# Optimization experiments

Measured on AMD Instinct MI355X. Metric: run time of the kernel, lower is better.

The kernel has to match this reference:

```python
import jax, jax.numpy as jnp
import numpy as np
from jax import lax

YXS = [(100, 250), (250, 250), (400, 250)]
HWS = [(50, 400), (50, 400), (50, 400)]
RATIO = 0.8
RCNN_THRES = 0.25
YOLO_THRES = 0.45
NMS_THRES = 0.4


def setup_inputs() -> dict:
    key = jax.random.key(0)
    ks = jax.random.split(key, 6)
    img = jax.random.uniform(ks[0], (1, 3, 500, 500), dtype=jnp.float32)
    patch0 = jax.random.normal(ks[1], (3, 50, 400), dtype=jnp.float32)
    patch1 = jax.random.normal(ks[2], (3, 50, 400), dtype=jnp.float32)
    patch2 = jax.random.normal(ks[3], (3, 50, 400), dtype=jnp.float32)
    rcnn_probs = jax.random.uniform(ks[4], (6144, 81), dtype=jnp.float32)
    boxes = jax.random.uniform(ks[5], (6144, 6), dtype=jnp.float32)
    return {"img": img, "patch0": patch0, "patch1": patch1, "patch2": patch2,
            "rcnn_probs": rcnn_probs, "boxes": boxes}


def _iou_matrix(b):
    # b: [M,4] center format (x, y, w, h) -> pairwise IoU [M,M]
    x1 = b[:, 0] - b[:, 2] * 0.5
    x2 = b[:, 0] + b[:, 2] * 0.5
    y1 = b[:, 1] - b[:, 3] * 0.5
    y2 = b[:, 1] + b[:, 3] * 0.5
    iw = jnp.maximum(jnp.minimum(x2[:, None], x2[None, :]) - jnp.maximum(x1[:, None], x1[None, :]), 0.0)
    ih = jnp.maximum(jnp.minimum(y2[:, None], y2[None, :]) - jnp.maximum(y1[:, None], y1[None, :]), 0.0)
    inter = iw * ih
    area = b[:, 2] * b[:, 3]
    union = area[:, None] + area[None, :] - inter
    return inter / jnp.maximum(union, 1e-12)


def _box_loss(c5, c4, mask):
    # per-box clamp/log loss on cls_conf (c5) and det_conf (c4), masked sum
    s = 1.0 / (0.5 - YOLO_THRES)
    l = (-jnp.clip((c5 - YOLO_THRES) * s, 0.0, 1.0) * jnp.log(1.0 - c5 + 0.01)
         - jnp.clip((c4 - YOLO_THRES) * s, 0.0, 1.0) * jnp.log(1.0 - c4 + 0.01))
    return jnp.sum(jnp.where(mask, l, 0.0))


def reference(img, patch0, patch1, patch2, rcnn_probs, boxes):
    # --- patch blending ---
    for (y, x), (h, w), p in zip(YXS, HWS, (patch0, patch1, patch2)):
        img = img.at[0, :, y - h // 2:y - h // 2 + h, x - w // 2:x - w // 2 + w].add(p)
    # clamp-violation penalty: (-img[img<0]).sum() + (img[img>1]-1).sum()
    p_loss = jnp.sum(jnp.maximum(-img, 0.0)) + jnp.sum(jnp.maximum(img - 1.0, 0.0))
    img = jnp.clip(img, 0.0, 1.0)

    # --- rcnn postprocessing loss ---
    prob = jnp.max(rcnn_probs[:, :-1], axis=-1)
    rmask = prob > RCNN_THRES
    b_prob = rcnn_probs[:, -1]
    r_loss = -jnp.sum(jnp.where(rmask, jnp.log(b_prob + 0.001), 0.0))
    r_loss += -jnp.sum(jnp.where(rmask,
                                 jnp.clip((prob - RCNN_THRES) / (0.3 - RCNN_THRES), 0.0, 1.0)
                                 * jnp.log(1.0 - prob + 0.001), 0.0))

    # --- yolo per-box loss + greedy IoU-NMS loss ---
    conf = boxes[:, 4]
    valid = conf > YOLO_THRES
    b_loss = _box_loss(boxes[:, 5], conf, valid)

    M = boxes.shape[0]
    order = jnp.argsort(-conf)
    sb = boxes[order]          # sorted by det_conf desc
    sv = valid[order]
    iou = _iou_matrix(sb[:, :4])  # [M,M]
    idx = jnp.arange(M)

    def body(keep, i):
        sup = (iou[i] > NMS_THRES) & (idx > i) & keep[i]
        return keep & ~sup, None

    keep, _ = lax.scan(body, sv, idx)
    b_nms_loss = _box_loss(sb[:, 5], sb[:, 4], keep)

    b_cnt = jnp.sum(valid.astype(jnp.float32))
    b_nms_cnt = jnp.maximum(jnp.sum(keep.astype(jnp.float32)), 1.0)
    yolo_loss = b_loss + b_nms_loss * (b_cnt / b_nms_cnt)

    loss = r_loss * RATIO + yolo_loss + p_loss
    return loss
```

## Files before the change

### kernel.cpp

```cpp
#include <hip/hip_runtime.h>
#include <hip/hip_bf16.h>
#include <stdint.h>

#define RCNN_THRES 0.25f
#define YOLO_THRES 0.45f
#define NMS_THRES  0.4f

#define M_BOXES 6144
#define NWORDS  96
#define SORT_N  4096

#define RK_BLOCKS 96
#define PL_BLOCKS 733
#define RL_BLOCKS 384
#define BL_BLOCKS 6
#define P_ELEMS  750000
#define MB_BLOCKS 1024

typedef unsigned long long u64;

__device__ inline float wave_sum(float v) {
#pragma unroll
    for (int o = 32; o > 0; o >>= 1) v += __shfl_xor(v, o);
    return v;
}
__device__ inline float wave_max(float v) {
#pragma unroll
    for (int o = 32; o > 0; o >>= 1) v = fmaxf(v, __shfl_xor(v, o));
    return v;
}

__device__ inline u64 readlane_u64(u64 v, int l) {
    unsigned lo = (unsigned)__builtin_amdgcn_readlane((int)(unsigned)v, l);
    unsigned hi = (unsigned)__builtin_amdgcn_readlane((int)(unsigned)(v >> 32), l);
    return ((u64)hi << 32) | (u64)lo;
}

__device__ inline float box_loss_term(float c5, float c4) {
    float a = fminf(fmaxf((c5 - YOLO_THRES) * 20.0f, 0.0f), 1.0f);
    float b = fminf(fmaxf((c4 - YOLO_THRES) * 20.0f, 0.0f), 1.0f);
    return -a * logf(1.0f - c5 + 0.01f) - b * logf(1.0f - c4 + 0.01f);
}

__device__ inline bool iou_gt(float x1a, float y1a, float x2a, float y2a, float aa,
                              float x1b, float y1b, float x2b, float y2b, float ab) {
    float iw = fmaxf(fminf(x2a, x2b) - fmaxf(x1a, x1b), 0.0f);
    float ih = fmaxf(fminf(y2a, y2b) - fmaxf(y1a, y1b), 0.0f);
    float inter = iw * ih;
    float uni = aa + ab - inter;
    return (inter / fmaxf(uni, 1e-12f)) > NMS_THRES;
}

__device__ inline u64 vw_word(int w, int nv) {
    int rem = nv - (w << 6);
    if (rem >= 64) return ~0ull;
    if (rem <= 0) return 0ull;
    return (1ull << rem) - 1ull;
}

__global__ __launch_bounds__(1024) void sort_and_losses(
    const float* __restrict__ boxes,
    const float* __restrict__ img, const float* __restrict__ p0,
    const float* __restrict__ p1, const float* __restrict__ p2,
    const float* __restrict__ probs,
    float* __restrict__ sx1, float* __restrict__ sy1,
    float* __restrict__ sx2, float* __restrict__ sy2,
    float* __restrict__ sarea, float* __restrict__ sconf, float* __restrict__ sc5,
    int* __restrict__ nvp, float* __restrict__ acc) {
    const int bid = blockIdx.x;
    const int tid = threadIdx.x, lane = tid & 63, wid = tid >> 6;

    if (bid < RK_BLOCKS) {
        __shared__ u64 KL[M_BOXES];
        __shared__ float cred[16];
        float myvalid = 0.0f;
#pragma unroll
        for (int s = 0; s < 6; ++s) {
            int p = tid + s * 1024;
            float conf = boxes[p * 6 + 4];
            u64 key = 0ull;
            if (conf > YOLO_THRES) {
                key = ((u64)__float_as_uint(conf) << 13) | (u64)(8191 - p);
                myvalid += 1.0f;
            }
            KL[p] = key;
        }
        __syncthreads();
        if (bid == 0) {
            float c = wave_sum(myvalid);
            if (lane == 0) cred[wid] = c;
            __syncthreads();
            if (tid == 0) {
                float t = 0.0f;
#pragma unroll
                for (int k = 0; k < 16; ++k) t += cred[k];
                *nvp = (int)(t + 0.5f);
            }
        }
        const int box = bid * 64 + (tid >> 4);
        const int seg = tid & 15;
        const u64 mykey = KL[box];
        int cnt = 0;
        for (int i = seg; i < M_BOXES; i += 16)
            cnt += (KL[i] > mykey) ? 1 : 0;
#pragma unroll
        for (int o = 1; o < 16; o <<= 1) cnt += __shfl_xor(cnt, o);
        if (seg == 0 && mykey != 0ull) {
            int rank = cnt;
            if (rank < SORT_N) {
                const float* b6 = boxes + box * 6;
                float x = b6[0], y = b6[1], wd = b6[2], ht = b6[3];
                sx1[rank] = x - wd * 0.5f;
                sx2[rank] = x + wd * 0.5f;
                sy1[rank] = y - ht * 0.5f;
                sy2[rank] = y + ht * 0.5f;
                sarea[rank] = wd * ht;
                sconf[rank] = b6[4];
                sc5[rank] = b6[5];
            }
        }
        return;
    }

    __shared__ float fred[32];
    if (bid < RK_BLOCKS + PL_BLOCKS) {
        int e = (bid - RK_BLOCKS) * 1024 + tid;
        float local = 0.0f;
        if (e < P_ELEMS) {
            float v = img[e];
            int c = e / 250000;
            int rem = e - c * 250000;
            int y = rem / 500;
            int x = rem - y * 500;
            if (x >= 50 && x < 450) {
                int px = x - 50;
                if (y >= 75 && y < 125)       v += p0[c * 20000 + (y - 75) * 400 + px];
                else if (y >= 225 && y < 275) v += p1[c * 20000 + (y - 225) * 400 + px];
                else if (y >= 375 && y < 425) v += p2[c * 20000 + (y - 375) * 400 + px];
            }
            local = fmaxf(-v, 0.0f) + fmaxf(v - 1.0f, 0.0f);
        }
        local = wave_sum(local);
        if (lane == 0) fred[wid] = local;
        __syncthreads();
        if (tid == 0) {
            float t = 0.0f;
#pragma unroll
            for (int k = 0; k < 16; ++k) t += fred[k];
            atomicAdd(&acc[0], t);
        }
    } else if (bid < RK_BLOCKS + PL_BLOCKS + RL_BLOCKS) {
        int row = (bid - RK_BLOCKS - PL_BLOCKS) * 16 + wid;
        const float* pr = probs + row * 81;
        float m = pr[lane];
        if (lane < 16) m = fmaxf(m, pr[64 + lane]);
        m = wave_max(m);
        float t = 0.0f;
        if (lane == 0 && m > RCNN_THRES) {
            float bp = pr[80];
            float cl = fminf(fmaxf((m - RCNN_THRES) * (1.0f / (0.3f - RCNN_THRES)), 0.0f), 1.0f);
            t = -logf(bp + 0.001f) - cl * logf(1.0f - m + 0.001f);
        }
        if (lane == 0) fred[wid] = t;
        __syncthreads();
        if (tid == 0) {
            float s = 0.0f;
#pragma unroll
            for (int k = 0; k < 16; ++k) s += fred[k];
            atomicAdd(&acc[1], s);
        }
    } else {
        int i = (bid - RK_BLOCKS - PL_BLOCKS - RL_BLOCKS) * 1024 + tid;
        float l = 0.0f, cnt = 0.0f;
        if (i < M_BOXES) {
            float conf = boxes[i * 6 + 4];
            if (conf > YOLO_THRES) {
                l = box_loss_term(boxes[i * 6 + 5], conf);
                cnt = 1.0f;
            }
        }
        l = wave_sum(l);
        cnt = wave_sum(cnt);
        if (lane == 0) { fred[wid] = l; fred[16 + wid] = cnt; }
        __syncthreads();
        if (tid == 0) {
            float tl = 0.0f, tc = 0.0f;
#pragma unroll
            for (int k = 0; k < 16; ++k) { tl += fred[k]; tc += fred[16 + k]; }
            atomicAdd(&acc[2], tl);
            atomicAdd(&acc[3], tc);
        }
    }
}

__global__ __launch_bounds__(256) void build_mask(
    const float* __restrict__ sx1, const float* __restrict__ sy1,
    const float* __restrict__ sx2, const float* __restrict__ sy2,
    const float* __restrict__ sarea, const int* __restrict__ nvp,
    u64* __restrict__ mask) {
    const int lane = threadIdx.x & 63, wid = threadIdx.x >> 6;
    const int nv = *nvp;
    int row = blockIdx.x * 4 + wid;
    if (row >= nv) return;
    const int nwa = (nv + 63) >> 6;
    float rx1 = sx1[row], ry1 = sy1[row], rx2 = sx2[row], ry2 = sy2[row];
    float ra = sarea[row];
    u64* mrow = mask + (size_t)row * NWORDS;
    for (int w = row >> 6; w < nwa; ++w) {
        int j = w * 64 + lane;
        bool pred = (j > row) && (j < nv) &&
                    iou_gt(rx1, ry1, rx2, ry2, ra,
                           sx1[j], sy1[j], sx2[j], sy2[j], sarea[j]);
        u64 bits = __ballot(pred);
        if (lane == 0) mrow[w] = bits;
    }
}

__global__ __launch_bounds__(512) void nms_walk(
    const float* __restrict__ acc, const int* __restrict__ nvp,
    const u64* __restrict__ mask,
    const float* __restrict__ sconf, const float* __restrict__ sc5,
    float* __restrict__ out) {
    __shared__ u64 SLICE[2][1024];
    __shared__ u64 SUPC[8][NWORDS];
    __shared__ u64 KW[NWORDS];
    __shared__ float fred[16];

    const int tid = threadIdx.x, lane = tid & 63, wid = tid >> 6;
    const int nv = *nvp;
    const int nwa = (nv + 63) >> 6;
    const int ngrp = (nwa + 3) >> 2;

    for (int i = tid; i < 8 * NWORDS; i += 512) ((u64*)SUPC)[i] = 0ull;
    for (int i = tid; i < NWORDS; i += 512) KW[i] = 0ull;
    {
        int r = tid >> 1, h = tid & 1;
        ulonglong2 m = *(const ulonglong2*)(mask + (size_t)r * NWORDS + 2 * h);
        *(ulonglong2*)&SLICE[0][r * 4 + 2 * h] = m;
    }
    __syncthreads();

    for (int g = 0; g < ngrp; ++g) {
        const int W = 4 * g;
        const int buf = g & 1;

        ulonglong2 stg{};
        const bool do_stage = (g + 1 < ngrp);
        if (do_stage) {
            int r = tid >> 1, h = tid & 1;
            stg = *(const ulonglong2*)(mask +
                    (size_t)((g + 1) * 256 + r) * NWORDS + (4 * (g + 1) + 2 * h));
        }

        if (wid == 0) {
            const u64* SL = SLICE[buf];
            ulonglong2 S0lo = *(const ulonglong2*)&SL[(0 * 64 + lane) * 4];
            ulonglong2 S0hi = *(const ulonglong2*)&SL[(0 * 64 + lane) * 4 + 2];
            ulonglong2 S1lo = *(const ulonglong2*)&SL[(1 * 64 + lane) * 4];
            ulonglong2 S1hi = *(const ulonglong2*)&SL[(1 * 64 + lane) * 4 + 2];
            ulonglong2 S2hi = *(const ulonglong2*)&SL[(2 * 64 + lane) * 4 + 2];
            ulonglong2 S3hi = *(const ulonglong2*)&SL[(3 * 64 + lane) * 4 + 2];
            (void)S1lo;

            u64 supW0 = 0ull, supW1 = 0ull, supW2 = 0ull, supW3 = 0ull;
#pragma unroll
            for (int k = 0; k < 8; ++k) {
                ulonglong2 a = *(const ulonglong2*)&SUPC[k][W];
                ulonglong2 b = *(const ulonglong2*)&SUPC[k][W + 2];
                supW0 |= a.x; supW1 |= a.y; supW2 |= b.x; supW3 |= b.y;
            }

            u64 gs1 = 0ull, gs2 = 0ull, gs3 = 0ull;
            u64 vw, cur, rem;
            vw = vw_word(W + 0, nv);
            if (vw) {
                cur = vw & ~supW0; rem = cur;
                while (rem) {
                    int t = __builtin_amdgcn_readfirstlane((int)__builtin_ctzll(rem));
                    u64 d = readlane_u64(S0lo.x, t);
                    gs1 |= readlane_u64(S0lo.y, t);
                    gs2 |= readlane_u64(S0hi.x, t);
                    gs3 |= readlane_u64(S0hi.y, t);
                    cur &= ~d; rem &= ~d; rem &= rem - 1;
                }
                if (lane == 0) KW[W + 0] = cur;
            }
            vw = vw_word(W + 1, nv);
            if (vw) {
                cur = vw & ~(supW1 | gs1); rem = cur;
                while (rem) {
                    int t = __builtin_amdgcn_readfirstlane((int)__builtin_ctzll(rem));
                    u64 d = readlane_u64(S1lo.y, t);
                    gs2 |= readlane_u64(S1hi.x, t);
                    gs3 |= readlane_u64(S1hi.y, t);
                    cur &= ~d; rem &= ~d; rem &= rem - 1;
                }
                if (lane == 0) KW[W + 1] = cur;
            }
            vw = vw_word(W + 2, nv);
            if (vw) {
                cur = vw & ~(supW2 | gs2); rem = cur;
                while (rem) {
                    int t = __builtin_amdgcn_readfirstlane((int)__builtin_ctzll(rem));
                    u64 d = readlane_u64(S2hi.x, t);
                    gs3 |= readlane_u64(S2hi.y, t);
                    cur &= ~d; rem &= ~d; rem &= rem - 1;
                }
                if (lane == 0) KW[W + 2] = cur;
            }
            vw = vw_word(W + 3, nv);
            if (vw) {
                cur = vw & ~(supW3 | gs3); rem = cur;
                while (rem) {
                    int t = __builtin_amdgcn_readfirstlane((int)__builtin_ctzll(rem));
                    u64 d = readlane_u64(S3hi.y, t);
                    cur &= ~d; rem &= ~d; rem &= rem - 1;
                }
                if (lane == 0) KW[W + 3] = cur;
            }
        }
        __syncthreads();

        if (do_stage) {
            int r = tid >> 1, h = tid & 1;
            *(ulonglong2*)&SLICE[buf ^ 1][r * 4 + 2 * h] = stg;
        }

        const int Wp4 = W + 4;
        const int nwrem = NWORDS - Wp4;
        if (nwrem > 0) {
            u64 kw0 = KW[W], kw1 = KW[W + 1], kw2 = KW[W + 2], kw3 = KW[W + 3];
            int idx = 0, nmine = 0;
            int b0 = 0, b1 = 0, b2 = 0, b3 = 0;
            const bool lactive = (2 * lane) < nwrem;
            const u64* bp = mask + Wp4 + 2 * lane;
            u64* scrow = &SUPC[wid][0];
#pragma unroll
            for (int c = 0; c < 4; ++c) {
                u64 k = (c == 0) ? kw0 : (c == 1) ? kw1 : (c == 2) ? kw2 : kw3;
                while (k) {
                    int bpos = (int)__builtin_ctzll(k); k &= k - 1;
                    if ((idx & 7) == wid) {
                        int row = ((W + c) << 6) + bpos;
                        int sl = nmine & 3;
                        if (sl == 0) b0 = row;
                        else if (sl == 1) b1 = row;
                        else if (sl == 2) b2 = row;
                        else b3 = row;
                        nmine++;
                        if ((nmine & 3) == 0 && lactive) {
                            ulonglong2 m0 = *(const ulonglong2*)(bp + (size_t)b0 * NWORDS);
                            ulonglong2 m1 = *(const ulonglong2*)(bp + (size_t)b1 * NWORDS);
                            ulonglong2 m2 = *(const ulonglong2*)(bp + (size_t)b2 * NWORDS);
                            ulonglong2 m3 = *(const ulonglong2*)(bp + (size_t)b3 * NWORDS);
                            scrow[Wp4 + 2 * lane]     |= m0.x | m1.x | m2.x | m3.x;
                            scrow[Wp4 + 2 * lane + 1] |= m0.y | m1.y | m2.y | m3.y;
                        }
                    }
                    idx++;
                }
            }
            if ((nmine & 3) != 0 && lactive) {
                int n = nmine & 3;
                int a1 = (n > 1) ? b1 : b0, a2 = (n > 2) ? b2 : b0;
                ulonglong2 m0 = *(const ulonglong2*)(bp + (size_t)b0 * NWORDS);
                ulonglong2 m1 = *(const ulonglong2*)(bp + (size_t)a1 * NWORDS);
                ulonglong2 m2 = *(const ulonglong2*)(bp + (size_t)a2 * NWORDS);
                scrow[Wp4 + 2 * lane]     |= m0.x | m1.x | m2.x;
                scrow[Wp4 + 2 * lane + 1] |= m0.y | m1.y | m2.y;
            }
        }
        __syncthreads();
    }

    float nl = 0.0f, nc = 0.0f;
    for (int p = tid; p < M_BOXES; p += 512) {
        if ((KW[p >> 6] >> (p & 63)) & 1ull) {
            nl += box_loss_term(sc5[p], sconf[p]);
            nc += 1.0f;
        }
    }
    nl = wave_sum(nl);
    nc = wave_sum(nc);
    if (lane == 0) { fred[wid] = nl; fred[8 + wid] = nc; }
    __syncthreads();
    if (tid == 0) {
        float tnl = 0.0f, tnc = 0.0f;
#pragma unroll
        for (int k = 0; k < 8; ++k) { tnl += fred[k]; tnc += fred[8 + k]; }
        float p_loss = acc[0], r_loss = acc[1], b_loss = acc[2], b_cnt = acc[3];
        float yolo = b_loss + tnl * (b_cnt / fmaxf(tnc, 1.0f));
        out[0] = r_loss * 0.8f + yolo + p_loss;
    }
}

extern "C" void kernel_launch(void* const* d_in, const int* in_sizes, int n_in,
                              void* d_out, int out_size, void* d_ws, size_t ws_size,
                              hipStream_t stream) {
    const float* img   = (const float*)d_in[0];
    const float* p0    = (const float*)d_in[1];
    const float* p1    = (const float*)d_in[2];
    const float* p2    = (const float*)d_in[3];
    const float* probs = (const float*)d_in[4];
    const float* boxes = (const float*)d_in[5];
    float* out = (float*)d_out;

    char* ws = (char*)d_ws;
    float* acc = (float*)ws;
    int* nvp = (int*)(ws + 32);
    float* sx1 = (float*)(ws + 1024);
    float* sy1 = sx1 + M_BOXES;
    float* sx2 = sy1 + M_BOXES;
    float* sy2 = sx2 + M_BOXES;
    float* sarea = sy2 + M_BOXES;
    float* sconf = sarea + M_BOXES;
    float* sc5 = sconf + M_BOXES;
    u64* mask = (u64*)(ws + 173056);

    hipMemsetAsync(acc, 0, 64, stream);
    sort_and_losses<<<RK_BLOCKS + PL_BLOCKS + RL_BLOCKS + BL_BLOCKS, 1024, 0, stream>>>(
        boxes, img, p0, p1, p2, probs,
        sx1, sy1, sx2, sy2, sarea, sconf, sc5, nvp, acc);
    build_mask<<<MB_BLOCKS, 256, 0, stream>>>(sx1, sy1, sx2, sy2, sarea, nvp, mask);
    nms_walk<<<1, 512, 0, stream>>>(acc, nvp, mask, sconf, sc5, out);
}
```

Measured before the change: 157.9 us.

## Fuse mask build and NMS walk into one kernel with chunk-ready flags

```diff
diff --git a/kernel.cpp b/kernel.cpp
--- a/kernel.cpp
+++ b/kernel.cpp
@@ -15,7 +15,7 @@
 #define RL_BLOCKS 384
 #define BL_BLOCKS 6
 #define P_ELEMS  750000
-#define MB_BLOCKS 1024
+#define BW_BLOCKS 512
 
 typedef unsigned long long u64;
 
@@ -56,6 +56,11 @@
     if (rem >= 64) return ~0ull;
     if (rem <= 0) return 0ull;
     return (1ull << rem) - 1ull;
+}
+
+__device__ inline void wait_chunk(const int* cd, int c) {
+    while (__hip_atomic_load(cd + c, __ATOMIC_ACQUIRE, __HIP_MEMORY_SCOPE_AGENT) < 32)
+        __builtin_amdgcn_s_sleep(2);
 }
 
 __global__ __launch_bounds__(1024) void sort_and_losses(
@@ -193,46 +198,49 @@
     }
 }
 
-__global__ __launch_bounds__(256) void build_mask(
+__global__ __launch_bounds__(512) void build_and_walk(
+    const float* __restrict__ acc, const int* __restrict__ nvp,
     const float* __restrict__ sx1, const float* __restrict__ sy1,
     const float* __restrict__ sx2, const float* __restrict__ sy2,
-    const float* __restrict__ sarea, const int* __restrict__ nvp,
-    u64* __restrict__ mask) {
-    const int lane = threadIdx.x & 63, wid = threadIdx.x >> 6;
+    const float* __restrict__ sarea,
+    const float* __restrict__ sconf, const float* __restrict__ sc5,
+    u64* __restrict__ mask, int* __restrict__ chunkdone,
+    float* __restrict__ out) {
+    const int tid = threadIdx.x, lane = tid & 63, wid = tid >> 6;
     const int nv = *nvp;
-    int row = blockIdx.x * 4 + wid;
-    if (row >= nv) return;
     const int nwa = (nv + 63) >> 6;
-    float rx1 = sx1[row], ry1 = sy1[row], rx2 = sx2[row], ry2 = sy2[row];
-    float ra = sarea[row];
-    u64* mrow = mask + (size_t)row * NWORDS;
-    for (int w = row >> 6; w < nwa; ++w) {
-        int j = w * 64 + lane;
-        bool pred = (j > row) && (j < nv) &&
-                    iou_gt(rx1, ry1, rx2, ry2, ra,
-                           sx1[j], sy1[j], sx2[j], sy2[j], sarea[j]);
-        u64 bits = __ballot(pred);
-        if (lane == 0) mrow[w] = bits;
-    }
-}
-
-__global__ __launch_bounds__(512) void nms_walk(
-    const float* __restrict__ acc, const int* __restrict__ nvp,
-    const u64* __restrict__ mask,
-    const float* __restrict__ sconf, const float* __restrict__ sc5,
-    float* __restrict__ out) {
+
+    if (blockIdx.x < BW_BLOCKS) {
+        int row = blockIdx.x * 8 + wid;
+        if (row < nv) {
+            float rx1 = sx1[row], ry1 = sy1[row], rx2 = sx2[row], ry2 = sy2[row];
+            float ra = sarea[row];
+            u64* mrow = mask + (size_t)row * NWORDS;
+            for (int w = row >> 6; w < nwa; ++w) {
+                int j = w * 64 + lane;
+                bool pred = (j > row) && (j < nv) &&
+                            iou_gt(rx1, ry1, rx2, ry2, ra,
+                                   sx1[j], sy1[j], sx2[j], sy2[j], sarea[j]);
+                u64 bits = __ballot(pred);
+                if (lane == 0) mrow[w] = bits;
+            }
+        }
+        __threadfence();
+        __syncthreads();
+        if (tid == 0) atomicAdd(&chunkdone[blockIdx.x >> 5], 1);
+        return;
+    }
+
     __shared__ u64 SLICE[2][1024];
     __shared__ u64 SUPC[8][NWORDS];
     __shared__ u64 KW[NWORDS];
     __shared__ float fred[16];
 
-    const int tid = threadIdx.x, lane = tid & 63, wid = tid >> 6;
-    const int nv = *nvp;
-    const int nwa = (nv + 63) >> 6;
     const int ngrp = (nwa + 3) >> 2;
 
     for (int i = tid; i < 8 * NWORDS; i += 512) ((u64*)SUPC)[i] = 0ull;
     for (int i = tid; i < NWORDS; i += 512) KW[i] = 0ull;
+    wait_chunk(chunkdone, 0);
     {
         int r = tid >> 1, h = tid & 1;
         ulonglong2 m = *(const ulonglong2*)(mask + (size_t)r * NWORDS + 2 * h);
@@ -247,6 +255,7 @@
         ulonglong2 stg{};
         const bool do_stage = (g + 1 < ngrp);
         if (do_stage) {
+            wait_chunk(chunkdone, g + 1);
             int r = tid >> 1, h = tid & 1;
             stg = *(const ulonglong2*)(mask +
                     (size_t)((g + 1) * 256 + r) * NWORDS + (4 * (g + 1) + 2 * h));
@@ -408,6 +417,7 @@
     char* ws = (char*)d_ws;
     float* acc = (float*)ws;
     int* nvp = (int*)(ws + 32);
+    int* chunkdone = (int*)(ws + 128);
     float* sx1 = (float*)(ws + 1024);
     float* sy1 = sx1 + M_BOXES;
     float* sx2 = sy1 + M_BOXES;
@@ -417,10 +427,10 @@
     float* sc5 = sconf + M_BOXES;
     u64* mask = (u64*)(ws + 173056);
 
-    hipMemsetAsync(acc, 0, 64, stream);
+    hipMemsetAsync(ws, 0, 256, stream);
     sort_and_losses<<<RK_BLOCKS + PL_BLOCKS + RL_BLOCKS + BL_BLOCKS, 1024, 0, stream>>>(
         boxes, img, p0, p1, p2, probs,
         sx1, sy1, sx2, sy2, sarea, sconf, sc5, nvp, acc);
-    build_mask<<<MB_BLOCKS, 256, 0, stream>>>(sx1, sy1, sx2, sy2, sarea, nvp, mask);
-    nms_walk<<<1, 512, 0, stream>>>(acc, nvp, mask, sconf, sc5, out);
-}
+    build_and_walk<<<BW_BLOCKS + 1, 512, 0, stream>>>(
+        acc, nvp, sx1, sy1, sx2, sy2, sarea, sconf, sc5, mask, chunkdone, out);
+}
```

New measurement: 292.0 us. 1.85x slower.
